# Performance work log

Hardware: AMD Instinct MI355X
Metric: run time of the kernel (lower is better)

## Reference

```python
import jax, jax.numpy as jnp
import numpy as np

N_NODES = 50000
N_EDGES = 800000
NUM_GRAPHS = 512
IN_DIM = 128
HID = 128
OUT_DIM = 1


def setup_inputs() -> dict:
    key = jax.random.key(0)
    ks = jax.random.split(key, 8)
    x = jax.random.normal(ks[0], (N_NODES, IN_DIM), dtype=jnp.float32)
    edge_index = jax.random.randint(ks[1], (2, N_EDGES), 0, N_NODES, dtype=jnp.int64)
    batch = jnp.sort(jax.random.randint(ks[2], (N_NODES,), 0, NUM_GRAPHS, dtype=jnp.int64))
    s1 = 1.0 / np.sqrt(IN_DIM)
    s2 = 1.0 / np.sqrt(HID)
    W1 = jax.random.normal(ks[3], (IN_DIM, HID), dtype=jnp.float32) * s1
    b1 = jnp.zeros((HID,), dtype=jnp.float32)
    W2 = jax.random.normal(ks[4], (HID, HID), dtype=jnp.float32) * s2
    b2 = jnp.zeros((HID,), dtype=jnp.float32)
    Wl = jax.random.normal(ks[5], (HID, OUT_DIM), dtype=jnp.float32) * s2
    bl = jnp.zeros((OUT_DIM,), dtype=jnp.float32)
    return {"x": x, "edge_index": edge_index, "batch": batch,
            "W1": W1, "b1": b1, "W2": W2, "b2": b2, "Wl": Wl, "bl": bl}


def _gcn_conv(x, src, dst, norm, W, b):
    # GCNConv: D^{-1/2}(A+I)D^{-1/2} X W + b (self-loops already in src/dst)
    h = x @ W                                    # [N, H]
    msg = h[src] * norm[:, None]                 # gather + edge-normalize
    agg = jax.ops.segment_sum(msg, dst, num_segments=N_NODES)  # scatter-add
    return agg + b


def reference(x, edge_index, batch, W1, b1, W2, b2, Wl, bl):
    loops = jnp.arange(N_NODES, dtype=edge_index.dtype)
    src = jnp.concatenate([edge_index[0], loops])
    dst = jnp.concatenate([edge_index[1], loops])
    deg = jax.ops.segment_sum(jnp.ones_like(dst, dtype=x.dtype), dst, num_segments=N_NODES)
    dinv = jax.lax.rsqrt(deg)                    # deg >= 1 due to self-loops
    norm = dinv[src] * dinv[dst]                 # symmetric normalization per edge

    h = jax.nn.relu(_gcn_conv(x, src, dst, norm, W1, b1))
    h = jax.nn.relu(_gcn_conv(h, src, dst, norm, W2, b2))

    # global_mean_pool over graph ids
    sums = jax.ops.segment_sum(h, batch, num_segments=NUM_GRAPHS)
    cnts = jax.ops.segment_sum(jnp.ones((N_NODES,), dtype=h.dtype), batch, num_segments=NUM_GRAPHS)
    pooled = sums / jnp.maximum(cnts, 1.0)[:, None]

    out = jax.nn.sigmoid(pooled @ Wl + bl)       # [G, 1]
    return out.squeeze(1)                        # [G]
```

## Files before the change

### kernel.cpp

```cpp
#include <hip/hip_runtime.h>
#include <hip/hip_bf16.h>

#define N_NODES 50000
#define N_EDGES 800000
#define NUM_GRAPHS 512
#define MAXDEG 64
#define EPB 4096
#define P1_BLOCKS 196
#define NBUCK 256
#define NPB 196

typedef short short8 __attribute__((ext_vector_type(8)));
typedef unsigned short u16x8 __attribute__((ext_vector_type(8)));
typedef float f32x4 __attribute__((ext_vector_type(4)));

__device__ __forceinline__ unsigned short f2bu(float f) {
    __hip_bfloat16 h = __float2bfloat16(f);
    return *reinterpret_cast<unsigned short*>(&h);
}
__device__ __forceinline__ float bu2f(unsigned short u) {
    unsigned int v = ((unsigned int)u) << 16;
    float f;
    __builtin_memcpy(&f, &v, 4);
    return f;
}

__global__ __launch_bounds__(256) void bin_k(const int* __restrict__ ei,
                                             unsigned int* __restrict__ staging,
                                             int* __restrict__ cnts_tbl,
                                             int* __restrict__ offs_tbl,
                                             unsigned short* __restrict__ hs1,
                                             unsigned short* __restrict__ hs2) {
    __shared__ unsigned int st[EPB];
    __shared__ int cnt[NBUCK], cur[NBUCK], scan[NBUCK];
    int b = blockIdx.x, t = threadIdx.x;
    if (b == 0 && t < 64)
        ((unsigned int*)(hs1 + (size_t)N_NODES * 128))[t] = 0u;
    if (b == 1 && t < 64)
        ((unsigned int*)(hs2 + (size_t)N_NODES * 128))[t] = 0u;
    cnt[t] = 0;
    __syncthreads();

    int e0 = b * EPB;
    int srcv[16], dstv[16], bk[16];
#pragma unroll
    for (int k = 0; k < 16; ++k) {
        int e = e0 + k * 256 + t;
        bool ok = e < N_EDGES;
        srcv[k] = ok ? ei[e] : 0;
        dstv[k] = ok ? ei[N_EDGES + e] : 0;
        bk[k] = ok ? (dstv[k] / NPB) : -1;
        if (ok) atomicAdd(&cnt[bk[k]], 1);
    }
    __syncthreads();
    scan[t] = cnt[t];
    __syncthreads();
    for (int off = 1; off < 256; off <<= 1) {
        int u = t >= off ? scan[t - off] : 0;
        __syncthreads();
        scan[t] += u;
        __syncthreads();
    }
    int excl = scan[t] - cnt[t];
    cur[t] = excl;
    cnts_tbl[t * P1_BLOCKS + b] = cnt[t];
    offs_tbl[t * P1_BLOCKS + b] = excl;
    __syncthreads();
#pragma unroll
    for (int k = 0; k < 16; ++k) {
        if (bk[k] >= 0) {
            int pos = atomicAdd(&cur[bk[k]], 1);
            int dl = dstv[k] - bk[k] * NPB;
            st[pos] = (unsigned int)srcv[k] | ((unsigned int)dl << 16);
        }
    }
    __syncthreads();
    unsigned int* gout = staging + (size_t)b * EPB;
    for (int i = t; i < EPB; i += 256) gout[i] = st[i];
}

__global__ __launch_bounds__(256) void adjbuild_k(const unsigned int* __restrict__ staging,
                                                  const int* __restrict__ cnts_tbl,
                                                  const int* __restrict__ offs_tbl,
                                                  unsigned short* __restrict__ adj,
                                                  int* __restrict__ cnt,
                                                  float* __restrict__ dinv,
                                                  const float* __restrict__ W1,
                                                  const float* __restrict__ W2,
                                                  unsigned short* __restrict__ W1t,
                                                  unsigned short* __restrict__ W2t) {
    int b = blockIdx.x, t = threadIdx.x;
    if (b >= NBUCK) {
        int wb = b - NBUCK;
        const float* W = wb < 64 ? W1 : W2;
        unsigned short* Wt = wb < 64 ? W1t : W2t;
        int idx = (wb & 63) * 256 + t;
        int k = idx >> 7, n = idx & 127;
        Wt[n * 128 + k] = f2bu(W[idx]);
        return;
    }
    __shared__ unsigned short adjL[NPB * MAXDEG];
    __shared__ int cntL[NPB];
    __shared__ int segStart[P1_BLOCKS + 1];
    __shared__ int segOff[P1_BLOCKS];
    __shared__ int tmp[256];

    if (t < NPB) cntL[t] = 0;
    int c = t < P1_BLOCKS ? cnts_tbl[b * P1_BLOCKS + t] : 0;
    if (t < P1_BLOCKS) segOff[t] = offs_tbl[b * P1_BLOCKS + t];
    tmp[t] = c;
    __syncthreads();
    for (int off = 1; off < 256; off <<= 1) {
        int u = t >= off ? tmp[t - off] : 0;
        __syncthreads();
        tmp[t] += u;
        __syncthreads();
    }
    if (t < P1_BLOCKS) segStart[t] = tmp[t] - c;
    if (t == 0) segStart[P1_BLOCKS] = tmp[P1_BLOCKS - 1];
    __syncthreads();

    int T = segStart[P1_BLOCKS];
    for (int f = t; f < T; f += 256) {
        int lo = 0, hi = P1_BLOCKS;
        while (hi - lo > 1) {
            int m = (lo + hi) >> 1;
            if (segStart[m] <= f) lo = m; else hi = m;
        }
        unsigned int p = staging[(size_t)lo * EPB + segOff[lo] + (f - segStart[lo])];
        int src = p & 0xFFFF;
        int dl = p >> 16;
        int slot = atomicAdd(&cntL[dl], 1);
        if (slot < MAXDEG - 1) adjL[dl * MAXDEG + slot] = (unsigned short)src;
    }
    __syncthreads();

    int nodeBase = b * NPB;
    if (t < NPB) {
        int node = nodeBase + t;
        int cc = cntL[t];
        int ec = cc < MAXDEG - 1 ? cc : MAXDEG - 1;
        adjL[t * MAXDEG + ec] = (unsigned short)node;
        int tot = ec + 1, tot4 = (tot + 3) & ~3;
        for (int s = tot; s < tot4; ++s) adjL[t * MAXDEG + s] = (unsigned short)N_NODES;
        if (node < N_NODES) {
            cnt[node] = tot4;
            dinv[node] = rsqrtf((float)cc + 1.0f);
        }
    }
    __syncthreads();
    unsigned int* g = (unsigned int*)(adj + (size_t)nodeBase * MAXDEG);
    const unsigned int* l = (const unsigned int*)adjL;
    for (int i = t; i < NPB * MAXDEG / 2; i += 256) g[i] = l[i];
}

template <bool F32A>
__global__ __launch_bounds__(256) void gemm_k(const void* __restrict__ Ap,
                                              const unsigned short* __restrict__ Wt,
                                              const float* __restrict__ dinv,
                                              unsigned short* __restrict__ C) {
    __shared__ unsigned short Wl[128 * 136];
    int t = threadIdx.x;
    for (int idx = t; idx < 2048; idx += 256) {
        int n = idx >> 4, c = idx & 15;
        *(u16x8*)(Wl + n * 136 + c * 8) = *(const u16x8*)(Wt + n * 128 + c * 8);
    }
    __syncthreads();

    int wave = t >> 6, lane = t & 63, quad = lane >> 4, ln = lane & 15;
    int rb = blockIdx.x * 128 + wave * 16;

    short8 a[2][4];
#pragma unroll
    for (int mt = 0; mt < 2; ++mt) {
        int r = rb + mt * 64 + ln;
        r = r < N_NODES ? r : N_NODES - 1;
        if (F32A) {
            const float* arow = (const float*)Ap + (size_t)r * 128 + quad * 8;
#pragma unroll
            for (int ks = 0; ks < 4; ++ks) {
                float4 v0 = *(const float4*)(arow + ks * 32);
                float4 v1 = *(const float4*)(arow + ks * 32 + 4);
                short8 av;
                av[0] = (short)f2bu(v0.x); av[1] = (short)f2bu(v0.y);
                av[2] = (short)f2bu(v0.z); av[3] = (short)f2bu(v0.w);
                av[4] = (short)f2bu(v1.x); av[5] = (short)f2bu(v1.y);
                av[6] = (short)f2bu(v1.z); av[7] = (short)f2bu(v1.w);
                a[mt][ks] = av;
            }
        } else {
            const unsigned short* arow = (const unsigned short*)Ap + (size_t)r * 128 + quad * 8;
#pragma unroll
            for (int ks = 0; ks < 4; ++ks) a[mt][ks] = *(const short8*)(arow + ks * 32);
        }
    }

    f32x4 acc[2][8];
#pragma unroll
    for (int mt = 0; mt < 2; ++mt)
#pragma unroll
        for (int ct = 0; ct < 8; ++ct) acc[mt][ct] = (f32x4){0.f, 0.f, 0.f, 0.f};

#pragma unroll
    for (int ks = 0; ks < 4; ++ks)
#pragma unroll
        for (int ct = 0; ct < 8; ++ct) {
            short8 b = *(const short8*)(Wl + (ct * 16 + ln) * 136 + ks * 32 + quad * 8);
            acc[0][ct] = __builtin_amdgcn_mfma_f32_16x16x32_bf16(a[0][ks], b, acc[0][ct], 0, 0, 0);
            acc[1][ct] = __builtin_amdgcn_mfma_f32_16x16x32_bf16(a[1][ks], b, acc[1][ct], 0, 0, 0);
        }

#pragma unroll
    for (int mt = 0; mt < 2; ++mt) {
#pragma unroll
        for (int rr = 0; rr < 4; ++rr) {
            int r = rb + mt * 64 + quad * 4 + rr;
            if (r >= N_NODES) continue;
            float dv = dinv[r];
#pragma unroll
            for (int ct = 0; ct < 8; ++ct)
                C[(size_t)r * 128 + ct * 16 + ln] = f2bu(acc[mt][ct][rr] * dv);
        }
    }
}

__global__ __launch_bounds__(256) void agg1_k(const unsigned short* __restrict__ hs,
                                              const unsigned short* __restrict__ adj,
                                              const int* __restrict__ cnt,
                                              const float* __restrict__ dinv,
                                              const float* __restrict__ bias,
                                              unsigned short* __restrict__ out) {
    int t = threadIdx.x;
    int wave = t >> 6, lane = t & 63, quad = lane >> 4, fl = lane & 15;
    int node = blockIdx.x * 16 + wave * 4 + quad;
    int2 pack = ((const int2*)(adj + (size_t)node * MAXDEG))[fl];
    int rounds = cnt[node] >> 2;
    float dv = dinv[node];
    float4 b0 = *(const float4*)(bias + fl * 8);
    float4 b1 = *(const float4*)(bias + fl * 8 + 4);
    int qb = quad << 4;

    float a[8];
#pragma unroll
    for (int j = 0; j < 8; ++j) a[j] = 0.f;

    int i = 0;
    for (; i + 2 <= rounds; i += 2) {
        unsigned pAx = (unsigned)__shfl(pack.x, qb + i, 64);
        unsigned pAy = (unsigned)__shfl(pack.y, qb + i, 64);
        unsigned pBx = (unsigned)__shfl(pack.x, qb + i + 1, 64);
        unsigned pBy = (unsigned)__shfl(pack.y, qb + i + 1, 64);
        u16x8 v0 = *(const u16x8*)(hs + (size_t)(pAx & 0xFFFFu) * 128 + fl * 8);
        u16x8 v1 = *(const u16x8*)(hs + (size_t)(pAx >> 16) * 128 + fl * 8);
        u16x8 v2 = *(const u16x8*)(hs + (size_t)(pAy & 0xFFFFu) * 128 + fl * 8);
        u16x8 v3 = *(const u16x8*)(hs + (size_t)(pAy >> 16) * 128 + fl * 8);
        u16x8 v4 = *(const u16x8*)(hs + (size_t)(pBx & 0xFFFFu) * 128 + fl * 8);
        u16x8 v5 = *(const u16x8*)(hs + (size_t)(pBx >> 16) * 128 + fl * 8);
        u16x8 v6 = *(const u16x8*)(hs + (size_t)(pBy & 0xFFFFu) * 128 + fl * 8);
        u16x8 v7 = *(const u16x8*)(hs + (size_t)(pBy >> 16) * 128 + fl * 8);
#pragma unroll
        for (int j = 0; j < 8; ++j)
            a[j] += ((bu2f(v0[j]) + bu2f(v1[j])) + (bu2f(v2[j]) + bu2f(v3[j])))
                  + ((bu2f(v4[j]) + bu2f(v5[j])) + (bu2f(v6[j]) + bu2f(v7[j])));
    }
    if (i < rounds) {
        unsigned px = (unsigned)__shfl(pack.x, qb + i, 64);
        unsigned py = (unsigned)__shfl(pack.y, qb + i, 64);
        u16x8 v0 = *(const u16x8*)(hs + (size_t)(px & 0xFFFFu) * 128 + fl * 8);
        u16x8 v1 = *(const u16x8*)(hs + (size_t)(px >> 16) * 128 + fl * 8);
        u16x8 v2 = *(const u16x8*)(hs + (size_t)(py & 0xFFFFu) * 128 + fl * 8);
        u16x8 v3 = *(const u16x8*)(hs + (size_t)(py >> 16) * 128 + fl * 8);
#pragma unroll
        for (int j = 0; j < 8; ++j)
            a[j] += (bu2f(v0[j]) + bu2f(v1[j])) + (bu2f(v2[j]) + bu2f(v3[j]));
    }

    u16x8 o;
    o[0] = f2bu(fmaxf(a[0] * dv + b0.x, 0.f));
    o[1] = f2bu(fmaxf(a[1] * dv + b0.y, 0.f));
    o[2] = f2bu(fmaxf(a[2] * dv + b0.z, 0.f));
    o[3] = f2bu(fmaxf(a[3] * dv + b0.w, 0.f));
    o[4] = f2bu(fmaxf(a[4] * dv + b1.x, 0.f));
    o[5] = f2bu(fmaxf(a[5] * dv + b1.y, 0.f));
    o[6] = f2bu(fmaxf(a[6] * dv + b1.z, 0.f));
    o[7] = f2bu(fmaxf(a[7] * dv + b1.w, 0.f));
    *(u16x8*)(out + (size_t)node * 128 + fl * 8) = o;
}

__global__ __launch_bounds__(256) void agg_dot_k(const unsigned short* __restrict__ hs,
                                                 const unsigned short* __restrict__ adj,
                                                 const int* __restrict__ cnt,
                                                 const float* __restrict__ dinv,
                                                 const float* __restrict__ bias,
                                                 const float* __restrict__ Wl,
                                                 float* __restrict__ pnode) {
    int t = threadIdx.x;
    int wave = t >> 6, lane = t & 63, quad = lane >> 4, fl = lane & 15;
    int node = blockIdx.x * 16 + wave * 4 + quad;
    int2 pack = ((const int2*)(adj + (size_t)node * MAXDEG))[fl];
    int rounds = cnt[node] >> 2;
    float dv = dinv[node];
    float4 b0 = *(const float4*)(bias + fl * 8);
    float4 b1 = *(const float4*)(bias + fl * 8 + 4);
    float4 w0 = *(const float4*)(Wl + fl * 8);
    float4 w1 = *(const float4*)(Wl + fl * 8 + 4);
    int qb = quad << 4;

    float a[8];
#pragma unroll
    for (int j = 0; j < 8; ++j) a[j] = 0.f;

    int i = 0;
    for (; i + 2 <= rounds; i += 2) {
        unsigned pAx = (unsigned)__shfl(pack.x, qb + i, 64);
        unsigned pAy = (unsigned)__shfl(pack.y, qb + i, 64);
        unsigned pBx = (unsigned)__shfl(pack.x, qb + i + 1, 64);
        unsigned pBy = (unsigned)__shfl(pack.y, qb + i + 1, 64);
        u16x8 v0 = *(const u16x8*)(hs + (size_t)(pAx & 0xFFFFu) * 128 + fl * 8);
        u16x8 v1 = *(const u16x8*)(hs + (size_t)(pAx >> 16) * 128 + fl * 8);
        u16x8 v2 = *(const u16x8*)(hs + (size_t)(pAy & 0xFFFFu) * 128 + fl * 8);
        u16x8 v3 = *(const u16x8*)(hs + (size_t)(pAy >> 16) * 128 + fl * 8);
        u16x8 v4 = *(const u16x8*)(hs + (size_t)(pBx & 0xFFFFu) * 128 + fl * 8);
        u16x8 v5 = *(const u16x8*)(hs + (size_t)(pBx >> 16) * 128 + fl * 8);
        u16x8 v6 = *(const u16x8*)(hs + (size_t)(pBy & 0xFFFFu) * 128 + fl * 8);
        u16x8 v7 = *(const u16x8*)(hs + (size_t)(pBy >> 16) * 128 + fl * 8);
#pragma unroll
        for (int j = 0; j < 8; ++j)
            a[j] += ((bu2f(v0[j]) + bu2f(v1[j])) + (bu2f(v2[j]) + bu2f(v3[j])))
                  + ((bu2f(v4[j]) + bu2f(v5[j])) + (bu2f(v6[j]) + bu2f(v7[j])));
    }
    if (i < rounds) {
        unsigned px = (unsigned)__shfl(pack.x, qb + i, 64);
        unsigned py = (unsigned)__shfl(pack.y, qb + i, 64);
        u16x8 v0 = *(const u16x8*)(hs + (size_t)(px & 0xFFFFu) * 128 + fl * 8);
        u16x8 v1 = *(const u16x8*)(hs + (size_t)(px >> 16) * 128 + fl * 8);
        u16x8 v2 = *(const u16x8*)(hs + (size_t)(py & 0xFFFFu) * 128 + fl * 8);
        u16x8 v3 = *(const u16x8*)(hs + (size_t)(py >> 16) * 128 + fl * 8);
#pragma unroll
        for (int j = 0; j < 8; ++j)
            a[j] += (bu2f(v0[j]) + bu2f(v1[j])) + (bu2f(v2[j]) + bu2f(v3[j]));
    }

    float p = fmaxf(a[0] * dv + b0.x, 0.f) * w0.x
            + fmaxf(a[1] * dv + b0.y, 0.f) * w0.y
            + fmaxf(a[2] * dv + b0.z, 0.f) * w0.z
            + fmaxf(a[3] * dv + b0.w, 0.f) * w0.w
            + fmaxf(a[4] * dv + b1.x, 0.f) * w1.x
            + fmaxf(a[5] * dv + b1.y, 0.f) * w1.y
            + fmaxf(a[6] * dv + b1.z, 0.f) * w1.z
            + fmaxf(a[7] * dv + b1.w, 0.f) * w1.w;
    p += __shfl_xor(p, 1, 64);
    p += __shfl_xor(p, 2, 64);
    p += __shfl_xor(p, 4, 64);
    p += __shfl_xor(p, 8, 64);
    if (fl == 0) pnode[node] = p;
}

__device__ __forceinline__ int lb(const int* a, int n, int v) {
    int lo = 0, hi = n;
    while (lo < hi) {
        int m = (lo + hi) >> 1;
        if (a[m] < v) lo = m + 1;
        else hi = m;
    }
    return lo;
}

__global__ __launch_bounds__(64) void final_k(const float* __restrict__ pnode,
                                              const int* __restrict__ batch,
                                              const float* __restrict__ bl,
                                              float* __restrict__ out) {
    int g = blockIdx.x, t = threadIdx.x;
    int lo = lb(batch, N_NODES, g), hi = lb(batch, N_NODES, g + 1);
    float s = 0.f;
    for (int r = lo + t; r < hi; r += 64) s += pnode[r];
#pragma unroll
    for (int o = 32; o > 0; o >>= 1) s += __shfl_down(s, o, 64);
    if (t == 0) {
        float cf = (float)(hi - lo);
        float z = s / fmaxf(cf, 1.f) + bl[0];
        out[g] = 1.f / (1.f + expf(-z));
    }
}

extern "C" void kernel_launch(void* const* d_in, const int* in_sizes, int n_in,
                              void* d_out, int out_size, void* d_ws, size_t ws_size,
                              hipStream_t stream) {
    const float* x = (const float*)d_in[0];
    const int* ei = (const int*)d_in[1];
    const int* batch = (const int*)d_in[2];
    const float* W1 = (const float*)d_in[3];
    const float* b1 = (const float*)d_in[4];
    const float* W2 = (const float*)d_in[5];
    const float* b2 = (const float*)d_in[6];
    const float* Wl = (const float*)d_in[7];
    const float* bl = (const float*)d_in[8];
    float* out = (float*)d_out;

    char* ws = (char*)d_ws;
    unsigned int* staging = (unsigned int*)(ws + 0x0);
    int* cnts_tbl = (int*)(ws + 0x310000);
    int* offs_tbl = (int*)(ws + 0x341000);
    unsigned short* adj = (unsigned short*)(ws + 0x372000);
    int* cnt = (int*)(ws + 0x992000);
    float* dinv = (float*)(ws + 0x9C3000);
    unsigned short* W1t = (unsigned short*)(ws + 0x9F4000);
    unsigned short* W2t = (unsigned short*)(ws + 0x9FC000);
    float* pnode = (float*)(ws + 0xA04000);
    unsigned short* hs1 = (unsigned short*)(ws + 0xA36000);
    unsigned short* h1 = (unsigned short*)(ws + 0x1672000);
    unsigned short* hs2 = (unsigned short*)(ws + 0x22AE000);

    bin_k<<<P1_BLOCKS, 256, 0, stream>>>(ei, staging, cnts_tbl, offs_tbl, hs1, hs2);
    adjbuild_k<<<NBUCK + 128, 256, 0, stream>>>(staging, cnts_tbl, offs_tbl,
                                                adj, cnt, dinv, W1, W2, W1t, W2t);

    gemm_k<true><<<(N_NODES + 127) / 128, 256, 0, stream>>>(x, W1t, dinv, hs1);
    agg1_k<<<N_NODES / 16, 256, 0, stream>>>(hs1, adj, cnt, dinv, b1, h1);
    gemm_k<false><<<(N_NODES + 127) / 128, 256, 0, stream>>>(h1, W2t, dinv, hs2);
    agg_dot_k<<<N_NODES / 16, 256, 0, stream>>>(hs2, adj, cnt, dinv, b2, Wl, pnode);

    final_k<<<NUM_GRAPHS, 64, 0, stream>>>(pnode, batch, bl, out);
}
```

Before: 190.6 us.

## Reorder second GCN layer to aggregate first, then fuse GEMM into aggregation

Uses associativity (A·H)·W2 = A·(H·W2) to aggregate the 128-wide layer-1 output (pre-scaled by dinv in agg1) directly, then multiplies the 16-node aggregated tile by W2 with MFMA inside the same kernel and reduces against Wl. This removes the separate second GEMM launch and the write and read of the hs2 intermediate. In exchange, each block re-reads W2t from global or cache, adds shared-memory staging and two barriers, and rounds the aggregated sum to bf16 before the matmul.

```diff
diff --git a/kernel.cpp b/kernel.cpp
--- a/kernel.cpp
+++ b/kernel.cpp
@@ -30,14 +30,14 @@
                                              int* __restrict__ cnts_tbl,
                                              int* __restrict__ offs_tbl,
                                              unsigned short* __restrict__ hs1,
-                                             unsigned short* __restrict__ hs2) {
+                                             unsigned short* __restrict__ h1) {
     __shared__ unsigned int st[EPB];
     __shared__ int cnt[NBUCK], cur[NBUCK], scan[NBUCK];
     int b = blockIdx.x, t = threadIdx.x;
     if (b == 0 && t < 64)
         ((unsigned int*)(hs1 + (size_t)N_NODES * 128))[t] = 0u;
     if (b == 1 && t < 64)
-        ((unsigned int*)(hs2 + (size_t)N_NODES * 128))[t] = 0u;
+        ((unsigned int*)(h1 + (size_t)N_NODES * 128))[t] = 0u;
     cnt[t] = 0;
     __syncthreads();
 
@@ -276,34 +276,34 @@
     }
 
     u16x8 o;
-    o[0] = f2bu(fmaxf(a[0] * dv + b0.x, 0.f));
-    o[1] = f2bu(fmaxf(a[1] * dv + b0.y, 0.f));
-    o[2] = f2bu(fmaxf(a[2] * dv + b0.z, 0.f));
-    o[3] = f2bu(fmaxf(a[3] * dv + b0.w, 0.f));
-    o[4] = f2bu(fmaxf(a[4] * dv + b1.x, 0.f));
-    o[5] = f2bu(fmaxf(a[5] * dv + b1.y, 0.f));
-    o[6] = f2bu(fmaxf(a[6] * dv + b1.z, 0.f));
-    o[7] = f2bu(fmaxf(a[7] * dv + b1.w, 0.f));
+    o[0] = f2bu(fmaxf(a[0] * dv + b0.x, 0.f) * dv);
+    o[1] = f2bu(fmaxf(a[1] * dv + b0.y, 0.f) * dv);
+    o[2] = f2bu(fmaxf(a[2] * dv + b0.z, 0.f) * dv);
+    o[3] = f2bu(fmaxf(a[3] * dv + b0.w, 0.f) * dv);
+    o[4] = f2bu(fmaxf(a[4] * dv + b1.x, 0.f) * dv);
+    o[5] = f2bu(fmaxf(a[5] * dv + b1.y, 0.f) * dv);
+    o[6] = f2bu(fmaxf(a[6] * dv + b1.z, 0.f) * dv);
+    o[7] = f2bu(fmaxf(a[7] * dv + b1.w, 0.f) * dv);
     *(u16x8*)(out + (size_t)node * 128 + fl * 8) = o;
 }
 
-__global__ __launch_bounds__(256) void agg_dot_k(const unsigned short* __restrict__ hs,
-                                                 const unsigned short* __restrict__ adj,
-                                                 const int* __restrict__ cnt,
-                                                 const float* __restrict__ dinv,
-                                                 const float* __restrict__ bias,
-                                                 const float* __restrict__ Wl,
-                                                 float* __restrict__ pnode) {
+__global__ __launch_bounds__(256) void agg2_fused_k(const unsigned short* __restrict__ hs,
+                                                    const unsigned short* __restrict__ adj,
+                                                    const int* __restrict__ cnt,
+                                                    const float* __restrict__ dinv,
+                                                    const float* __restrict__ bias,
+                                                    const unsigned short* __restrict__ W2t,
+                                                    const float* __restrict__ Wl,
+                                                    float* __restrict__ pnode) {
+    __shared__ unsigned short Az[16][136];
+    __shared__ float part[4][16];
     int t = threadIdx.x;
     int wave = t >> 6, lane = t & 63, quad = lane >> 4, fl = lane & 15;
-    int node = blockIdx.x * 16 + wave * 4 + quad;
+    int nl = wave * 4 + quad;
+    int node = blockIdx.x * 16 + nl;
     int2 pack = ((const int2*)(adj + (size_t)node * MAXDEG))[fl];
     int rounds = cnt[node] >> 2;
     float dv = dinv[node];
-    float4 b0 = *(const float4*)(bias + fl * 8);
-    float4 b1 = *(const float4*)(bias + fl * 8 + 4);
-    float4 w0 = *(const float4*)(Wl + fl * 8);
-    float4 w1 = *(const float4*)(Wl + fl * 8 + 4);
     int qb = quad << 4;
 
     float a[8];
@@ -341,19 +341,53 @@
             a[j] += (bu2f(v0[j]) + bu2f(v1[j])) + (bu2f(v2[j]) + bu2f(v3[j]));
     }
 
-    float p = fmaxf(a[0] * dv + b0.x, 0.f) * w0.x
-            + fmaxf(a[1] * dv + b0.y, 0.f) * w0.y
-            + fmaxf(a[2] * dv + b0.z, 0.f) * w0.z
-            + fmaxf(a[3] * dv + b0.w, 0.f) * w0.w
-            + fmaxf(a[4] * dv + b1.x, 0.f) * w1.x
-            + fmaxf(a[5] * dv + b1.y, 0.f) * w1.y
-            + fmaxf(a[6] * dv + b1.z, 0.f) * w1.z
-            + fmaxf(a[7] * dv + b1.w, 0.f) * w1.w;
-    p += __shfl_xor(p, 1, 64);
-    p += __shfl_xor(p, 2, 64);
-    p += __shfl_xor(p, 4, 64);
-    p += __shfl_xor(p, 8, 64);
-    if (fl == 0) pnode[node] = p;
+    u16x8 zv;
+#pragma unroll
+    for (int j = 0; j < 8; ++j) zv[j] = f2bu(a[j] * dv);
+    *(u16x8*)(&Az[nl][fl * 8]) = zv;
+    __syncthreads();
+
+    short8 af[4];
+#pragma unroll
+    for (int ks = 0; ks < 4; ++ks)
+        af[ks] = *(const short8*)(&Az[fl][ks * 32 + quad * 8]);
+
+    f32x4 acc[2];
+    acc[0] = (f32x4){0.f, 0.f, 0.f, 0.f};
+    acc[1] = (f32x4){0.f, 0.f, 0.f, 0.f};
+#pragma unroll
+    for (int ks = 0; ks < 4; ++ks)
+#pragma unroll
+        for (int ct = 0; ct < 2; ++ct) {
+            short8 b = *(const short8*)(W2t + (size_t)(wave * 32 + ct * 16 + fl) * 128 + ks * 32 + quad * 8);
+            acc[ct] = __builtin_amdgcn_mfma_f32_16x16x32_bf16(af[ks], b, acc[ct], 0, 0, 0);
+        }
+
+    float p[4];
+#pragma unroll
+    for (int rr = 0; rr < 4; ++rr) {
+        float s = 0.f;
+#pragma unroll
+        for (int ct = 0; ct < 2; ++ct) {
+            int col = wave * 32 + ct * 16 + fl;
+            s += fmaxf(acc[ct][rr] + bias[col], 0.f) * Wl[col];
+        }
+        p[rr] = s;
+    }
+#pragma unroll
+    for (int rr = 0; rr < 4; ++rr) {
+        p[rr] += __shfl_xor(p[rr], 1, 64);
+        p[rr] += __shfl_xor(p[rr], 2, 64);
+        p[rr] += __shfl_xor(p[rr], 4, 64);
+        p[rr] += __shfl_xor(p[rr], 8, 64);
+    }
+    if (fl == 0) {
+#pragma unroll
+        for (int rr = 0; rr < 4; ++rr) part[wave][quad * 4 + rr] = p[rr];
+    }
+    __syncthreads();
+    if (t < 16)
+        pnode[blockIdx.x * 16 + t] = part[0][t] + part[1][t] + part[2][t] + part[3][t];
 }
 
 __device__ __forceinline__ int lb(const int* a, int n, int v) {
@@ -409,16 +443,14 @@
     float* pnode = (float*)(ws + 0xA04000);
     unsigned short* hs1 = (unsigned short*)(ws + 0xA36000);
     unsigned short* h1 = (unsigned short*)(ws + 0x1672000);
-    unsigned short* hs2 = (unsigned short*)(ws + 0x22AE000);
-
-    bin_k<<<P1_BLOCKS, 256, 0, stream>>>(ei, staging, cnts_tbl, offs_tbl, hs1, hs2);
+
+    bin_k<<<P1_BLOCKS, 256, 0, stream>>>(ei, staging, cnts_tbl, offs_tbl, hs1, h1);
     adjbuild_k<<<NBUCK + 128, 256, 0, stream>>>(staging, cnts_tbl, offs_tbl,
                                                 adj, cnt, dinv, W1, W2, W1t, W2t);
 
     gemm_k<true><<<(N_NODES + 127) / 128, 256, 0, stream>>>(x, W1t, dinv, hs1);
     agg1_k<<<N_NODES / 16, 256, 0, stream>>>(hs1, adj, cnt, dinv, b1, h1);
-    gemm_k<false><<<(N_NODES + 127) / 128, 256, 0, stream>>>(h1, W2t, dinv, hs2);
-    agg_dot_k<<<N_NODES / 16, 256, 0, stream>>>(hs2, adj, cnt, dinv, b2, Wl, pnode);
+    agg2_fused_k<<<N_NODES / 16, 256, 0, stream>>>(h1, adj, cnt, dinv, b2, W2t, Wl, pnode);
 
     final_k<<<NUM_GRAPHS, 64, 0, stream>>>(pnode, batch, bl, out);
 }
```

Result: faster. 184.6 us (-3.1%).
